# Kernel tuning notes

Measured on AMD Instinct MI355X. Metric: run time of the kernel, lower is better.

The kernel has to match this reference:

```python
import jax, jax.numpy as jnp
import numpy as np
from jax import lax

B = 2048
C = 8
H = W = 14
NP = H * W  # 196
DIM = 192
THETA = 0.7


def _unfold3(z):
    # z: [B, C, H, W] -> patches [B, C, 9, H, W], matching F.unfold(kernel=3, pad=1)
    p = jnp.pad(z, ((0, 0), (0, 0), (1, 1), (1, 1)))
    return jnp.stack([p[:, :, dy:dy + H, dx:dx + W]
                      for dy in range(3) for dx in range(3)], axis=2)


def setup_inputs() -> dict:
    key = jax.random.key(0)
    ks = jax.random.split(key, 10)
    s = 0.1
    return {
        "x": jax.random.normal(ks[0], (B, 1 + NP, DIM), dtype=jnp.float32),
        "W1": jax.random.normal(ks[1], (C, DIM), dtype=jnp.float32) * s,      # linear1 192->8
        "b1": jax.random.normal(ks[2], (C,), dtype=jnp.float32) * s,
        "conv1_w": jax.random.normal(ks[3], (C, C), dtype=jnp.float32) * s,   # 1x1 conv
        "conv1_b": jax.random.normal(ks[4], (C,), dtype=jnp.float32) * s,
        "cdc_w": jax.random.normal(ks[5], (C, C, 1, 5), dtype=jnp.float32) * s,
        "wc1": jax.random.normal(ks[6], (C, C), dtype=jnp.float32) * s,       # WConv1 (1x1)
        "wc2": jax.random.normal(ks[7], (C, C), dtype=jnp.float32) * s,       # WConv2 (1x1)
        "hist_w": jax.random.normal(ks[8], (DIM, C), dtype=jnp.float32) * s,  # linear 8->192
        "hist_b": jax.random.normal(ks[9], (DIM,), dtype=jnp.float32) * s,
    }


def reference(x, W1, b1, conv1_w, conv1_b, cdc_w, wc1, wc2, hist_w, hist_b):
    class_token, tok = x[:, :1, :], x[:, 1:, :]
    # linear1: [B,196,192] -> [B,196,8]
    t = jnp.einsum('bnd,cd->bnc', tok, W1) + b1
    # -> [B,8,14,14]
    t = t.reshape(-1, H, W, C).transpose(0, 3, 1, 2)

    # conv1 (1x1)
    x1 = jnp.einsum('bihw,oi->bohw', t, conv1_w) + conv1_b[None, :, None, None]

    # CDC: scatter the 1x5 weights into a 3x3 cross-shaped kernel
    w5 = cdc_w[:, :, 0, :]  # [O,I,5]
    z = jnp.zeros((C, C, 1), dtype=cdc_w.dtype)
    k9 = jnp.concatenate([z, w5[:, :, 0:1], z,
                          w5[:, :, 1:2], w5[:, :, 2:3], w5[:, :, 3:4],
                          z, w5[:, :, 4:5], z], axis=2).reshape(C, C, 3, 3)
    out_normal = lax.conv_general_dilated(
        t, k9, window_strides=(1, 1), padding=((1, 1), (1, 1)),
        dimension_numbers=('NCHW', 'OIHW', 'NCHW'))
    kernel_diff = cdc_w.sum(axis=(2, 3))  # [O,I]
    out_diff = jnp.einsum('bihw,oi->bohw', t, kernel_diff)
    x2 = out_normal - THETA * out_diff

    z_star = x1 + x2  # [B,8,14,14]

    # TokenHistogram
    mu = jnp.einsum('bihw,oi->bohw', z_star, wc1)
    gamma = jnp.einsum('bihw,oi->bohw', z_star, wc2)
    zp = _unfold3(z_star)   # [B,8,9,14,14]
    mp = _unfold3(mu)
    gp = _unfold3(gamma)
    u = gp * (zp - mp)
    z_hist = jnp.exp(-u * u).sum(axis=2) / 9.0  # [B,8,14,14]
    # torch .reshape(-1, NP, 8): plain row-major reshape (mixes C and HW)
    z_hist = z_hist.reshape(-1, NP, C)
    y = jnp.einsum('bnc,dc->bnd', z_hist, hist_w) + hist_b  # [B,196,192]

    return jnp.concatenate([class_token, y], axis=1)
```

## Files before the change

kernel.cpp:

```cpp
#include <hip/hip_runtime.h>


#define NTOK 196
#define DIMD 192
#define CCH  8

__launch_bounds__(256, 4)
__global__ void sadapter_kernel(
    const float* __restrict__ x,
    const float* __restrict__ W1,
    const float* __restrict__ b1,
    const float* __restrict__ conv1_w,
    const float* __restrict__ conv1_b,
    const float* __restrict__ cdc_w,
    const float* __restrict__ wc1,
    const float* __restrict__ wc2,
    const float* __restrict__ hist_w,
    const float* __restrict__ hist_b,
    float* __restrict__ out)
{
    __shared__ float smem[9568];
    float* W1S   = smem;
    float* TOKC  = smem + 1568;
    float* ZS    = smem;
    float* PS    = smem + 2048;
    float* ZH    = smem + 4096;
    float* TS    = smem + 7056;
    float* HWT   = smem + 7056;
    float* HISTB = smem + 8592;
    float* WB    = smem + 9104;
    float* wCn = WB, *wU = WB+64, *wL = WB+128, *wR = WB+192, *wD = WB+256;
    float* wc1s = WB+320, *wc2s = WB+384;
    float* conv1bs = WB+448, *b1s = WB+456;

    const int tid = threadIdx.x;
    const int b = blockIdx.x;
    const float* xb  = x   + (size_t)b * (197*192);
    float*       outb = out + (size_t)b * (197*192);

    for (int f = tid; f < 512; f += 256) ((float4*)TS)[f] = make_float4(0.f,0.f,0.f,0.f);
    for (int f = tid; f < 384; f += 256) {
        int c = f / 48, d4 = f - c*48;
        ((float4*)W1S)[c*49 + d4] = ((const float4*)W1)[f];
    }
    if (tid < 64) {
        int o = tid >> 3, i = tid & 7;
        const float* c5 = cdc_w + o*40 + i*5;
        float k0=c5[0], k1=c5[1], k2=c5[2], k3=c5[3], k4=c5[4];
        float kd = k0+k1+k2+k3+k4;
        wU[tid]=k0; wL[tid]=k1; wR[tid]=k3; wD[tid]=k4;
        wCn[tid] = conv1_w[tid] + k2 - 0.7f*kd;
        wc1s[tid] = wc1[tid]; wc2s[tid] = wc2[tid];
    }
    if (tid < 8) { conv1bs[tid] = conv1_b[tid]; b1s[tid] = b1[tid]; }
    __syncthreads();

    const float* tokg = xb + DIMD;
    for (int k = 0; k < 7; ++k) {
        const float4* src = (const float4*)(tokg + k*(28*DIMD));
        for (int f = tid; f < 1344; f += 256) {
            float4 v = src[f];
            int n = f / 48, d4 = f - n*48;
            ((float4*)TOKC)[n*49 + d4] = v;
        }
        __syncthreads();
        if (tid < 224) {
            int nl = tid >> 3, c = tid & 7;
            const float4* tr = (const float4*)(TOKC + nl*196);
            const float4* wr = (const float4*)(W1S + c*196);
            float acc = b1s[c];
            #pragma unroll 8
            for (int d4 = 0; d4 < 48; ++d4) {
                float4 tv = tr[d4], wv = wr[d4];
                acc += tv.x*wv.x + tv.y*wv.y + tv.z*wv.z + tv.w*wv.w;
            }
            int n = k*28 + nl;
            int h = n / 14, w = n - h*14;
            TS[c*256 + (h+1)*16 + (w+1)] = acc;
        }
        __syncthreads();
    }

    for (int f = tid; f < 2048; f += 256) {
        int c = f >> 8, idx = f & 255, h = idx >> 4, w = idx & 15;
        float v = 0.f;
        if (h >= 1 && h <= 14 && w >= 1 && w <= 14) {
            float acc = conv1bs[c];
            #pragma unroll
            for (int i = 0; i < 8; ++i) {
                const float* tb = TS + i*256 + h*16 + w;
                int wi = c*8 + i;
                acc += wCn[wi]*tb[0] + wU[wi]*tb[-16] + wD[wi]*tb[16]
                     + wL[wi]*tb[-1] + wR[wi]*tb[1];
            }
            v = acc;
        }
        ZS[f] = v;
    }
    __syncthreads();

    for (int f = tid; f < 1536; f += 256) {
        int d = f >> 3, c = f & 7;
        HWT[c*DIMD + d] = hist_w[f];
    }
    if (tid < DIMD) HISTB[tid] = hist_b[tid];
    for (int f = tid; f < 2048; f += 256) {
        int c = f >> 8, idx = f & 255, h = idx >> 4, w = idx & 15;
        float v = 1.f;
        if (h >= 1 && h <= 14 && w >= 1 && w <= 14) {
            float zc = ZS[f];
            float mu = 0.f, ga = 0.f;
            #pragma unroll
            for (int i = 0; i < 8; ++i) {
                float zi = ZS[i*256 + idx];
                mu += wc1s[c*8+i]*zi;
                ga += wc2s[c*8+i]*zi;
            }
            float e = ga * (zc - mu);
            v = __expf(-e*e);
        }
        PS[f] = v;
    }
    __syncthreads();

    for (int f = tid; f < 1568; f += 256) {
        int c = f / 196, hw = f - c*196;
        int h = hw / 14, w = hw - h*14;
        const float* Pr = PS + c*256 + h*16 + w;
        float s9 = Pr[0]+Pr[1]+Pr[2] + Pr[16]+Pr[17]+Pr[18] + Pr[32]+Pr[33]+Pr[34];
        ZH[f] = s9 * (1.f/9.f);
    }
    __syncthreads();

    if (tid < 48) ((float4*)outb)[tid] = ((const float4*)xb)[tid];
    float4* outy = (float4*)(outb + DIMD);
    for (int j = tid; j < 9408; j += 256) {
        int n2 = j / 48, d4 = j - n2*48;
        float4 acc = ((const float4*)HISTB)[d4];
        const float* zr = ZH + n2*8;
        #pragma unroll
        for (int c2 = 0; c2 < 8; ++c2) {
            float s = zr[c2];
            float4 hv = ((const float4*)(HWT + c2*DIMD))[d4];
            acc.x += s*hv.x; acc.y += s*hv.y; acc.z += s*hv.z; acc.w += s*hv.w;
        }
        outy[j] = acc;
    }
}

extern "C" void kernel_launch(void* const* d_in, const int* in_sizes, int n_in,
                              void* d_out, int out_size, void* d_ws, size_t ws_size,
                              hipStream_t stream)
{
    const float* x       = (const float*)d_in[0];
    const float* W1      = (const float*)d_in[1];
    const float* b1      = (const float*)d_in[2];
    const float* conv1_w = (const float*)d_in[3];
    const float* conv1_b = (const float*)d_in[4];
    const float* cdc_w   = (const float*)d_in[5];
    const float* wc1     = (const float*)d_in[6];
    const float* wc2     = (const float*)d_in[7];
    const float* hist_w  = (const float*)d_in[8];
    const float* hist_b  = (const float*)d_in[9];
    float* out = (float*)d_out;

    sadapter_kernel<<<2048, 256, 0, stream>>>(
        x, W1, b1, conv1_w, conv1_b, cdc_w, wc1, wc2, hist_w, hist_b, out);
}
```

Baseline: 173.1 us.

## Restructure per-token stages to register-resident rows and cut shared memory

Each thread now takes one token. It computes the 192->8 linear projection with x loaded straight from global memory into registers and W1 read from global or cache, which removes the 7-step shared-memory token staging and its barriers. The conv, mu/gamma and exp stages are fused per token in registers, so the intermediate Z buffer is gone. Shared memory drops from about 38KB to about 25KB and launch bounds rise to 6 blocks per CU for more occupancy. The risks are uncoalesced per-thread row loads of x, since each thread streams a contiguous 768B row, and higher register pressure.

```diff
diff --git a/kernel.cpp b/kernel.cpp
--- a/kernel.cpp
+++ b/kernel.cpp
@@ -1,11 +1,9 @@
 #include <hip/hip_runtime.h>
 
 
-#define NTOK 196
 #define DIMD 192
-#define CCH  8
 
-__launch_bounds__(256, 4)
+__launch_bounds__(256, 6)
 __global__ void sadapter_kernel(
     const float* __restrict__ x,
     const float* __restrict__ W1,
@@ -19,132 +17,150 @@
     const float* __restrict__ hist_b,
     float* __restrict__ out)
 {
-    __shared__ float smem[9568];
-    float* W1S   = smem;
-    float* TOKC  = smem + 1568;
-    float* ZS    = smem;
+    __shared__ float smem[6176];
+    float* TS    = smem;
+    float* HWT   = smem;
+    float* HISTB = smem + 1536;
     float* PS    = smem + 2048;
     float* ZH    = smem + 4096;
-    float* TS    = smem + 7056;
-    float* HWT   = smem + 7056;
-    float* HISTB = smem + 8592;
-    float* WB    = smem + 9104;
-    float* wCn = WB, *wU = WB+64, *wL = WB+128, *wR = WB+192, *wD = WB+256;
-    float* wc1s = WB+320, *wc2s = WB+384;
-    float* conv1bs = WB+448, *b1s = WB+456;
+    float* WB2   = smem + 5664;
 
     const int tid = threadIdx.x;
-    const int b = blockIdx.x;
-    const float* xb  = x   + (size_t)b * (197*192);
-    float*       outb = out + (size_t)b * (197*192);
+    const float* xb   = x   + (size_t)blockIdx.x * (197 * DIMD);
+    float*       outb = out + (size_t)blockIdx.x * (197 * DIMD);
 
-    for (int f = tid; f < 512; f += 256) ((float4*)TS)[f] = make_float4(0.f,0.f,0.f,0.f);
-    for (int f = tid; f < 384; f += 256) {
-        int c = f / 48, d4 = f - c*48;
-        ((float4*)W1S)[c*49 + d4] = ((const float4*)W1)[f];
+    {
+        float4 z4 = make_float4(0.f, 0.f, 0.f, 0.f);
+        float4 o4 = make_float4(1.f, 1.f, 1.f, 1.f);
+        ((float4*)TS)[tid]       = z4;
+        ((float4*)TS)[tid + 256] = z4;
+        ((float4*)PS)[tid]       = o4;
+        ((float4*)PS)[tid + 256] = o4;
     }
     if (tid < 64) {
-        int o = tid >> 3, i = tid & 7;
-        const float* c5 = cdc_w + o*40 + i*5;
-        float k0=c5[0], k1=c5[1], k2=c5[2], k3=c5[3], k4=c5[4];
-        float kd = k0+k1+k2+k3+k4;
-        wU[tid]=k0; wL[tid]=k1; wR[tid]=k3; wD[tid]=k4;
-        wCn[tid] = conv1_w[tid] + k2 - 0.7f*kd;
-        wc1s[tid] = wc1[tid]; wc2s[tid] = wc2[tid];
-    }
-    if (tid < 8) { conv1bs[tid] = conv1_b[tid]; b1s[tid] = b1[tid]; }
-    __syncthreads();
-
-    const float* tokg = xb + DIMD;
-    for (int k = 0; k < 7; ++k) {
-        const float4* src = (const float4*)(tokg + k*(28*DIMD));
-        for (int f = tid; f < 1344; f += 256) {
-            float4 v = src[f];
-            int n = f / 48, d4 = f - n*48;
-            ((float4*)TOKC)[n*49 + d4] = v;
-        }
-        __syncthreads();
-        if (tid < 224) {
-            int nl = tid >> 3, c = tid & 7;
-            const float4* tr = (const float4*)(TOKC + nl*196);
-            const float4* wr = (const float4*)(W1S + c*196);
-            float acc = b1s[c];
-            #pragma unroll 8
-            for (int d4 = 0; d4 < 48; ++d4) {
-                float4 tv = tr[d4], wv = wr[d4];
-                acc += tv.x*wv.x + tv.y*wv.y + tv.z*wv.z + tv.w*wv.w;
-            }
-            int n = k*28 + nl;
-            int h = n / 14, w = n - h*14;
-            TS[c*256 + (h+1)*16 + (w+1)] = acc;
-        }
-        __syncthreads();
-    }
-
-    for (int f = tid; f < 2048; f += 256) {
-        int c = f >> 8, idx = f & 255, h = idx >> 4, w = idx & 15;
-        float v = 0.f;
-        if (h >= 1 && h <= 14 && w >= 1 && w <= 14) {
-            float acc = conv1bs[c];
-            #pragma unroll
-            for (int i = 0; i < 8; ++i) {
-                const float* tb = TS + i*256 + h*16 + w;
-                int wi = c*8 + i;
-                acc += wCn[wi]*tb[0] + wU[wi]*tb[-16] + wD[wi]*tb[16]
-                     + wL[wi]*tb[-1] + wR[wi]*tb[1];
-            }
-            v = acc;
-        }
-        ZS[f] = v;
+        const float* c5 = cdc_w + tid * 5;
+        float k0 = c5[0], k1 = c5[1], k2 = c5[2], k3 = c5[3], k4 = c5[4];
+        float kd = k0 + k1 + k2 + k3 + k4;
+        float* wp = WB2 + tid * 8;
+        wp[0] = conv1_w[tid] + k2 - 0.7f * kd;
+        wp[1] = k0;
+        wp[2] = k1;
+        wp[3] = k3;
+        wp[4] = k4;
+        wp[5] = wc1[tid];
+        wp[6] = wc2[tid];
+        wp[7] = 0.f;
     }
     __syncthreads();
 
-    for (int f = tid; f < 1536; f += 256) {
-        int d = f >> 3, c = f & 7;
-        HWT[c*DIMD + d] = hist_w[f];
+    if (tid < 196) {
+        const float4* rowp = (const float4*)(xb + DIMD + tid * DIMD);
+        float acc[8];
+        #pragma unroll
+        for (int c = 0; c < 8; ++c) acc[c] = b1[c];
+        #pragma unroll 2
+        for (int d8 = 0; d8 < 48; d8 += 8) {
+            float4 tv[8];
+            #pragma unroll
+            for (int u = 0; u < 8; ++u) tv[u] = rowp[d8 + u];
+            #pragma unroll
+            for (int u = 0; u < 8; ++u) {
+                const float* wp = W1 + (d8 + u) * 4;
+                #pragma unroll
+                for (int c = 0; c < 8; ++c) {
+                    acc[c] += tv[u].x * wp[c * DIMD + 0] + tv[u].y * wp[c * DIMD + 1]
+                            + tv[u].z * wp[c * DIMD + 2] + tv[u].w * wp[c * DIMD + 3];
+                }
+            }
+        }
+        int h = tid / 14, w = tid - h * 14;
+        float* tp = TS + (h + 1) * 16 + (w + 1);
+        #pragma unroll
+        for (int c = 0; c < 8; ++c) tp[c * 256] = acc[c];
+    } else if (tid >= 208) {
+        ((float4*)outb)[tid - 208] = ((const float4*)xb)[tid - 208];
     }
-    if (tid < DIMD) HISTB[tid] = hist_b[tid];
-    for (int f = tid; f < 2048; f += 256) {
-        int c = f >> 8, idx = f & 255, h = idx >> 4, w = idx & 15;
-        float v = 1.f;
-        if (h >= 1 && h <= 14 && w >= 1 && w <= 14) {
-            float zc = ZS[f];
+    __syncthreads();
+
+    if (tid < 196) {
+        int h = tid / 14, w = tid - h * 14;
+        const float* tp = TS + (h + 1) * 16 + (w + 1);
+        float zv[8];
+        #pragma unroll
+        for (int c = 0; c < 8; ++c) zv[c] = conv1_b[c];
+        #pragma unroll
+        for (int i = 0; i < 8; ++i) {
+            float t0 = tp[i * 256];
+            float tu = tp[i * 256 - 16];
+            float td = tp[i * 256 + 16];
+            float tl = tp[i * 256 - 1];
+            float tr = tp[i * 256 + 1];
+            #pragma unroll
+            for (int c = 0; c < 8; ++c) {
+                const float* wp = WB2 + (c * 8 + i) * 8;
+                float4 wv = *(const float4*)wp;
+                float wd = wp[4];
+                zv[c] += wv.x * t0 + wv.y * tu + wv.z * tl + wv.w * tr + wd * td;
+            }
+        }
+        float* pp = PS + (h + 1) * 16 + (w + 1);
+        #pragma unroll
+        for (int c = 0; c < 8; ++c) {
             float mu = 0.f, ga = 0.f;
             #pragma unroll
             for (int i = 0; i < 8; ++i) {
-                float zi = ZS[i*256 + idx];
-                mu += wc1s[c*8+i]*zi;
-                ga += wc2s[c*8+i]*zi;
+                const float* wp = WB2 + (c * 8 + i) * 8;
+                mu += wp[5] * zv[i];
+                ga += wp[6] * zv[i];
             }
-            float e = ga * (zc - mu);
-            v = __expf(-e*e);
+            float e = ga * (zv[c] - mu);
+            pp[c * 256] = __expf(-e * e);
         }
-        PS[f] = v;
     }
     __syncthreads();
 
-    for (int f = tid; f < 1568; f += 256) {
-        int c = f / 196, hw = f - c*196;
-        int h = hw / 14, w = hw - h*14;
-        const float* Pr = PS + c*256 + h*16 + w;
-        float s9 = Pr[0]+Pr[1]+Pr[2] + Pr[16]+Pr[17]+Pr[18] + Pr[32]+Pr[33]+Pr[34];
-        ZH[f] = s9 * (1.f/9.f);
+    if (tid < 196) {
+        int h = tid / 14, w = tid - h * 14;
+        const float* pb = PS + h * 16 + w;
+        #pragma unroll
+        for (int c = 0; c < 8; ++c) {
+            const float* pr = pb + c * 256;
+            float s9 = pr[0] + pr[1] + pr[2]
+                     + pr[16] + pr[17] + pr[18]
+                     + pr[32] + pr[33] + pr[34];
+            ZH[c * 196 + tid] = s9 * (1.f / 9.f);
+        }
+    } else {
+        for (int f = tid - 196; f < 384; f += 60) {
+            float4 v = ((const float4*)hist_w)[f];
+            int d = f >> 1, c0 = (f & 1) * 4;
+            HWT[(c0 + 0) * DIMD + d] = v.x;
+            HWT[(c0 + 1) * DIMD + d] = v.y;
+            HWT[(c0 + 2) * DIMD + d] = v.z;
+            HWT[(c0 + 3) * DIMD + d] = v.w;
+        }
+        for (int f = tid - 196; f < 48; f += 60)
+            ((float4*)HISTB)[f] = ((const float4*)hist_b)[f];
     }
     __syncthreads();
 
-    if (tid < 48) ((float4*)outb)[tid] = ((const float4*)xb)[tid];
-    float4* outy = (float4*)(outb + DIMD);
-    for (int j = tid; j < 9408; j += 256) {
-        int n2 = j / 48, d4 = j - n2*48;
-        float4 acc = ((const float4*)HISTB)[d4];
-        const float* zr = ZH + n2*8;
-        #pragma unroll
-        for (int c2 = 0; c2 < 8; ++c2) {
-            float s = zr[c2];
-            float4 hv = ((const float4*)(HWT + c2*DIMD))[d4];
-            acc.x += s*hv.x; acc.y += s*hv.y; acc.z += s*hv.z; acc.w += s*hv.w;
+    {
+        float4* outy = (float4*)(outb + DIMD);
+        int d4 = tid % 48;
+        int n2 = tid / 48;
+        while (n2 < 196) {
+            float4 a = ((const float4*)HISTB)[d4];
+            const float* zr = ZH + n2 * 8;
+            #pragma unroll
+            for (int c2 = 0; c2 < 8; ++c2) {
+                float s = zr[c2];
+                float4 hv = ((const float4*)(HWT + c2 * DIMD))[d4];
+                a.x += s * hv.x; a.y += s * hv.y; a.z += s * hv.z; a.w += s * hv.w;
+            }
+            outy[n2 * 48 + d4] = a;
+            n2 += 5; d4 += 16;
+            if (d4 >= 48) { d4 -= 48; n2 += 1; }
         }
-        outy[j] = acc;
     }
 }
 
```

After: 166.4 us. -3.9%, faster.
